# Optimization experiments

Hardware: AMD Instinct MI355X
Metric: run time of the kernel (lower is better)

## Reference

```python
import jax, jax.numpy as jnp
import numpy as np

N_NODES = 100000
N_EDGES = 1600000
IN_F = 128
OUT_F = 32
HEADS = 2
NEG_SLOPE = 0.2  # DGL GATConv default leaky_relu negative slope


def setup_inputs() -> dict:
    key = jax.random.key(0)
    ks = jax.random.split(key, 12)
    x = jax.random.normal(ks[0], (N_NODES, IN_F), dtype=jnp.float32)
    src = jax.random.randint(ks[1], (N_EDGES,), 0, N_NODES, dtype=jnp.int32)
    dst = jax.random.randint(ks[2], (N_EDGES,), 0, N_NODES, dtype=jnp.int32)
    # GATConv params: fc weight [IN_F, HEADS*OUT_F], attn_l/attn_r [HEADS, OUT_F], bias [HEADS*OUT_F]
    s = 1.0 / np.sqrt(IN_F)
    W = jax.random.normal(ks[3], (IN_F, HEADS * OUT_F), dtype=jnp.float32) * s
    attn_l = jax.random.normal(ks[4], (HEADS, OUT_F), dtype=jnp.float32) * s
    attn_r = jax.random.normal(ks[5], (HEADS, OUT_F), dtype=jnp.float32) * s
    bias_gat = jnp.zeros((HEADS * OUT_F,), dtype=jnp.float32)
    # MLPPredictor: lin1 (2*OUT_F -> OUT_F), lin2 (OUT_F -> 1)
    s1 = 1.0 / np.sqrt(2 * OUT_F)
    W1 = jax.random.normal(ks[6], (2 * OUT_F, OUT_F), dtype=jnp.float32) * s1
    b1 = jnp.zeros((OUT_F,), dtype=jnp.float32)
    s2 = 1.0 / np.sqrt(OUT_F)
    W2 = jax.random.normal(ks[7], (OUT_F, 1), dtype=jnp.float32) * s2
    b2 = jnp.zeros((1,), dtype=jnp.float32)
    return {"x": x, "W": W, "attn_l": attn_l, "attn_r": attn_r,
            "bias_gat": bias_gat, "W1": W1, "b1": b1, "W2": W2, "b2": b2,
            "src": src, "dst": dst}


def _forward(x, W, attn_l, attn_r, bias_gat, W1, b1, W2, b2, src, dst):
    # --- GATConv(in, out, 2 heads) ---
    feat = (x @ W).reshape(N_NODES, HEADS, OUT_F)           # [N,H,F]
    el = jnp.einsum('nhf,hf->nh', feat, attn_l)             # [N,H]
    er = jnp.einsum('nhf,hf->nh', feat, attn_r)             # [N,H]
    e = jax.nn.leaky_relu(el[src] + er[dst], NEG_SLOPE)     # [E,H]
    # edge softmax over incoming edges of each dst node (numerically stable)
    m = jax.ops.segment_max(e, dst, num_segments=N_NODES)   # [N,H]
    ex = jnp.exp(e - m[dst])                                # [E,H]
    denom = jax.ops.segment_sum(ex, dst, num_segments=N_NODES)  # [N,H]
    alpha = ex / denom[dst]                                 # [E,H]
    msg = feat[src] * alpha[:, :, None]                     # [E,H,F]
    rst = jax.ops.segment_sum(msg, dst, num_segments=N_NODES)   # [N,H,F]
    rst = rst + bias_gat.reshape(HEADS, OUT_F)
    h = jax.nn.relu(jnp.mean(rst, axis=1))                  # [N,F]
    # --- MLPPredictor: per-edge concat(src,dst) -> lin1 -> lin2 (no activation) ---
    hcat = jnp.concatenate([h[src], h[dst]], axis=1)        # [E,2F]
    score = (hcat @ W1 + b1) @ W2 + b2                      # [E,1]
    return score


def reference(x, W, attn_l, attn_r, bias_gat, W1, b1, W2, b2, src, dst):
    return _forward(x, W, attn_l, attn_r, bias_gat, W1, b1, W2, b2, src, dst)
```

## Files before the change

### kernel.cpp

```cpp
#include <hip/hip_runtime.h>
#include <hip/hip_fp16.h>

#define N_NODES 100000
#define N_EDGES 1600000
#define IN_F 128
#define OUT_F 32
#define HEADS 2
#define HO 64

#define NBUCK 782
#define BIN_BLOCKS 200
#define BIN_THREADS 1024
#define EPB (N_EDGES / BIN_BLOCKS)
#define CAP 36
#define LCAPH 1216

typedef __attribute__((ext_vector_type(8))) _Float16 half8;
typedef __attribute__((ext_vector_type(4))) _Float16 half4v;
typedef __attribute__((ext_vector_type(4))) float    f32x4;

#define XPAD 136

__global__ void wprep_k(const float* __restrict__ W,
                        const float* __restrict__ W1, const float* __restrict__ b1,
                        const float* __restrict__ W2, const float* __restrict__ b2,
                        _Float16* __restrict__ Wt16, float* __restrict__ wcomb,
                        float* __restrict__ ccomb){
  int tid = threadIdx.x;
  if (tid < HO){
    float a = 0.f;
    for (int k = 0; k < OUT_F; ++k) a = fmaf(W1[tid*OUT_F + k], W2[k], a);
    wcomb[tid] = a;
  }
  if (tid == HO){
    float a = 0.f;
    for (int k = 0; k < OUT_F; ++k) a = fmaf(b1[k], W2[k], a);
    *ccomb = a + b2[0];
  }
  for (int i = tid; i < 2048; i += 256){
    int k  = i >> 4;
    int c4 = (i & 15) * 4;
    float4 v = ((const float4*)W)[i];
    Wt16[(c4+0)*IN_F + k] = (_Float16)v.x;
    Wt16[(c4+1)*IN_F + k] = (_Float16)v.y;
    Wt16[(c4+2)*IN_F + k] = (_Float16)v.z;
    Wt16[(c4+3)*IN_F + k] = (_Float16)v.w;
  }
}

__global__ __launch_bounds__(256) void feat_k(
                       const float* __restrict__ x, const _Float16* __restrict__ Wt16,
                       const float* __restrict__ attn_l, const float* __restrict__ attn_r,
                       __half* __restrict__ feat16, float* __restrict__ el, float* __restrict__ er){
  __shared__ __align__(16) _Float16 Ws[64*XPAD];
  __shared__ __align__(16) _Float16 xs[64*XPAD];
  int tid = threadIdx.x;
  int node0 = blockIdx.x*64;

  for (int i = tid; i < 2048; i += 256){
    int c = i >> 5, k4 = i & 31;
    *(uint2*)&Ws[c*XPAD + k4*4] = ((const uint2*)Wt16)[i];
  }
  for (int i = tid; i < 2048; i += 256){
    int ln = i >> 5, kq = i & 31;
    int n = node0 + ln;
    float4 v = (n < N_NODES) ? ((const float4*)x)[(size_t)n*32 + kq]
                             : make_float4(0.f,0.f,0.f,0.f);
    half4v hv = { (_Float16)v.x, (_Float16)v.y, (_Float16)v.z, (_Float16)v.w };
    *(half4v*)&xs[ln*XPAD + kq*4] = hv;
  }
  __syncthreads();

  int w = tid >> 6, lane = tid & 63;
  int row_base = w*16;
  int lr = lane & 15, lg = lane >> 4;
  f32x4 acc0 = {0.f,0.f,0.f,0.f}, acc1 = {0.f,0.f,0.f,0.f};
  f32x4 acc2 = {0.f,0.f,0.f,0.f}, acc3 = {0.f,0.f,0.f,0.f};

  #pragma unroll
  for (int kk = 0; kk < 4; ++kk){
    int ko = kk*32 + lg*8;
    half8 a  = *(const half8*)&xs[(row_base + lr)*XPAD + ko];
    half8 b0 = *(const half8*)&Ws[( 0 + lr)*XPAD + ko];
    half8 b1 = *(const half8*)&Ws[(16 + lr)*XPAD + ko];
    half8 b2 = *(const half8*)&Ws[(32 + lr)*XPAD + ko];
    half8 b3 = *(const half8*)&Ws[(48 + lr)*XPAD + ko];
    acc0 = __builtin_amdgcn_mfma_f32_16x16x32_f16(a, b0, acc0, 0, 0, 0);
    acc1 = __builtin_amdgcn_mfma_f32_16x16x32_f16(a, b1, acc1, 0, 0, 0);
    acc2 = __builtin_amdgcn_mfma_f32_16x16x32_f16(a, b2, acc2, 0, 0, 0);
    acc3 = __builtin_amdgcn_mfma_f32_16x16x32_f16(a, b3, acc3, 0, 0, 0);
  }

  float al0 = attn_l[ 0 + lr], al1 = attn_l[16 + lr];
  float al2 = attn_l[32 + lr], al3 = attn_l[48 + lr];
  float ar0 = attn_r[ 0 + lr], ar1 = attn_r[16 + lr];
  float ar2 = attn_r[32 + lr], ar3 = attn_r[48 + lr];

  #pragma unroll
  for (int r = 0; r < 4; ++r){
    int n = node0 + row_base + lg*4 + r;
    float f0 = acc0[r], f1 = acc1[r], f2 = acc2[r], f3 = acc3[r];
    float p0 = f0*al0 + f1*al1, p1 = f2*al2 + f3*al3;
    float q0 = f0*ar0 + f1*ar1, q1 = f2*ar2 + f3*ar3;
    #pragma unroll
    for (int off = 1; off < 16; off <<= 1){
      p0 += __shfl_xor(p0, off); p1 += __shfl_xor(p1, off);
      q0 += __shfl_xor(q0, off); q1 += __shfl_xor(q1, off);
    }
    if (n < N_NODES){
      size_t base = (size_t)n*HO;
      feat16[base +  0 + lr] = __float2half_rn(f0);
      feat16[base + 16 + lr] = __float2half_rn(f1);
      feat16[base + 32 + lr] = __float2half_rn(f2);
      feat16[base + 48 + lr] = __float2half_rn(f3);
      if (lr == 0){
        *(float2*)&el[n*HEADS] = make_float2(p0, p1);
        *(float2*)&er[n*HEADS] = make_float2(q0, q1);
      }
    }
  }
}

__global__ void bin_k(const int* __restrict__ src, const int* __restrict__ dst,
                      const float* __restrict__ el, const float* __restrict__ er,
                      int* __restrict__ counts_t, uint2* __restrict__ stg){
  __shared__ int cnt[NBUCK];
  int tid = threadIdx.x, blk = blockIdx.x;
  for (int i = tid; i < NBUCK; i += BIN_THREADS) cnt[i] = 0;
  __syncthreads();
  const int4* s4p = (const int4*)(src + blk*EPB);
  const int4* d4p = (const int4*)(dst + blk*EPB);
  for (int i = tid; i < EPB/4; i += BIN_THREADS){
    int4 s4 = s4p[i];
    int4 d4 = d4p[i];
    int ss[4] = {s4.x, s4.y, s4.z, s4.w};
    int dd[4] = {d4.x, d4.y, d4.z, d4.w};
    #pragma unroll
    for (int u = 0; u < 4; ++u){
      int s = ss[u], d = dd[u];
      float2 elv = *(const float2*)&el[s*HEADS];
      float2 erv = *(const float2*)&er[d*HEADS];
      float t0 = elv.x + erv.x, t1 = elv.y + erv.y;
      t0 = t0 > 0.f ? t0 : 0.2f*t0;
      t1 = t1 > 0.f ? t1 : 0.2f*t1;
      __half2 ex2 = __float22half2_rn(make_float2(__expf(t0), __expf(t1)));
      int b = d >> 7;
      int slot = atomicAdd(&cnt[b], 1);
      if (slot < CAP)
        stg[((size_t)blk*NBUCK + b)*CAP + slot] =
          make_uint2(((unsigned int)s << 7) | (unsigned int)(d & 127),
                     *(const unsigned int*)&ex2);
    }
  }
  __syncthreads();
  for (int i = tid; i < NBUCK; i += BIN_THREADS)
    counts_t[i*BIN_BLOCKS + blk] = cnt[i] < CAP ? cnt[i] : CAP;
}

__global__ void __launch_bounds__(512, 8) scatter_agg_k(
                              const int* __restrict__ counts_t, const uint2* __restrict__ stg,
                              const __half* __restrict__ feat16, const float* __restrict__ bias,
                              const float* __restrict__ wcomb,
                              float* __restrict__ s1, float* __restrict__ s2){
  __shared__ uint2 lsev[LCAPH];
  __shared__ int cnts[BIN_BLOCKS];
  __shared__ int hist[64];
  __shared__ int start[64];
  __shared__ int cur[64];
  int bh = blockIdx.x;
  int b = bh >> 1, half = bh & 1;
  int tid = threadIdx.x;
  int w = tid >> 6, lane = tid & 63;
  if (tid < 64) hist[tid] = 0;
  for (int i = tid; i < BIN_BLOCKS; i += 512) cnts[i] = counts_t[b*BIN_BLOCKS + i];
  __syncthreads();

  int grp = tid >> 3, gl = tid & 7;

  for (int sg = grp; sg < BIN_BLOCKS; sg += 64){
    int n_seg = cnts[sg];
    const unsigned int* segx = (const unsigned int*)(stg + ((size_t)sg*NBUCK + b)*CAP);
    for (int j = gl; j < n_seg; j += 8){
      unsigned int rx = segx[2*j];
      int dl = rx & 127;
      if ((dl >> 6) == half) atomicAdd(&hist[dl & 63], 1);
    }
  }
  __syncthreads();

  if (tid < 64){
    int v = hist[tid];
    int inc = v;
    #pragma unroll
    for (int off = 1; off < 64; off <<= 1){
      int t = __shfl_up(inc, off);
      if (lane >= off) inc += t;
    }
    start[tid] = inc - v;
    cur[tid] = inc - v;
  }
  __syncthreads();

  for (int sg = grp; sg < BIN_BLOCKS; sg += 64){
    int n_seg = cnts[sg];
    const uint2* seg = stg + ((size_t)sg*NBUCK + b)*CAP;
    for (int j = gl; j < n_seg; j += 8){
      uint2 r = seg[j];
      int dl = r.x & 127;
      if ((dl >> 6) == half){
        int pos = atomicAdd(&cur[dl & 63], 1);
        if (pos < LCAPH) lsev[pos] = make_uint2(r.x >> 7, r.y);
      }
    }
  }
  __syncthreads();

  int g  = lane >> 4;
  int c4 = lane & 15;
  int h  = (c4 >= 8);
  float b0v = bias[c4*4 + 0], b1v = bias[c4*4 + 1], b2v = bias[c4*4 + 2], b3v = bias[c4*4 + 3];
  int f0 = (c4 & 7)*4;
  int wo = (h ? 32 : 0) + f0;
  float m0 = wcomb[wo], m1 = wcomb[wo+1], m2 = wcomb[wo+2], m3 = wcomb[wo+3];
  for (int i = 0; i < 8; ++i){
    int nl = w*8 + i;
    int node = bh*64 + nl;
    if (node >= N_NODES) break;
    int s0 = start[nl];
    int e0 = cur[nl]; if (e0 > LCAPH) e0 = LCAPH;
    int deg = e0 - s0; if (deg < 0) deg = 0;

    float a0=0.f, a1=0.f, a2=0.f, a3=0.f, dn=0.f;
    for (int j0 = 0; j0 < deg; j0 += 16){
      int jA = j0 + g, jB = j0 + 4 + g, jC = j0 + 8 + g, jD = j0 + 12 + g;
      float alA=0.f, alB=0.f, alC=0.f, alD=0.f;
      int snA=0, snB=0, snC=0, snD=0;
      if (jA < deg){ uint2 r = lsev[s0+jA]; snA = r.x;
        float2 e = __half22float2(*(const __half2*)&r.y); alA = (h?e.y:e.x); }
      if (jB < deg){ uint2 r = lsev[s0+jB]; snB = r.x;
        float2 e = __half22float2(*(const __half2*)&r.y); alB = (h?e.y:e.x); }
      if (jC < deg){ uint2 r = lsev[s0+jC]; snC = r.x;
        float2 e = __half22float2(*(const __half2*)&r.y); alC = (h?e.y:e.x); }
      if (jD < deg){ uint2 r = lsev[s0+jD]; snD = r.x;
        float2 e = __half22float2(*(const __half2*)&r.y); alD = (h?e.y:e.x); }
      dn += alA + alB + alC + alD;
      uint2 vA = *(const uint2*)(feat16 + (size_t)snA*HO + c4*4);
      uint2 vB = *(const uint2*)(feat16 + (size_t)snB*HO + c4*4);
      uint2 vC = *(const uint2*)(feat16 + (size_t)snC*HO + c4*4);
      uint2 vD = *(const uint2*)(feat16 + (size_t)snD*HO + c4*4);
      float2 fA01 = __half22float2(*(const __half2*)&vA.x);
      float2 fA23 = __half22float2(*(const __half2*)&vA.y);
      float2 fB01 = __half22float2(*(const __half2*)&vB.x);
      float2 fB23 = __half22float2(*(const __half2*)&vB.y);
      float2 fC01 = __half22float2(*(const __half2*)&vC.x);
      float2 fC23 = __half22float2(*(const __half2*)&vC.y);
      float2 fD01 = __half22float2(*(const __half2*)&vD.x);
      float2 fD23 = __half22float2(*(const __half2*)&vD.y);
      a0 = fmaf(alA, fA01.x, a0); a0 = fmaf(alB, fB01.x, a0);
      a0 = fmaf(alC, fC01.x, a0); a0 = fmaf(alD, fD01.x, a0);
      a1 = fmaf(alA, fA01.y, a1); a1 = fmaf(alB, fB01.y, a1);
      a1 = fmaf(alC, fC01.y, a1); a1 = fmaf(alD, fD01.y, a1);
      a2 = fmaf(alA, fA23.x, a2); a2 = fmaf(alB, fB23.x, a2);
      a2 = fmaf(alC, fC23.x, a2); a2 = fmaf(alD, fD23.x, a2);
      a3 = fmaf(alA, fA23.y, a3); a3 = fmaf(alB, fB23.y, a3);
      a3 = fmaf(alC, fC23.y, a3); a3 = fmaf(alD, fD23.y, a3);
    }
    a0 += __shfl_xor(a0, 16); a1 += __shfl_xor(a1, 16);
    a2 += __shfl_xor(a2, 16); a3 += __shfl_xor(a3, 16);
    dn += __shfl_xor(dn, 16);
    a0 += __shfl_xor(a0, 32); a1 += __shfl_xor(a1, 32);
    a2 += __shfl_xor(a2, 32); a3 += __shfl_xor(a3, 32);
    dn += __shfl_xor(dn, 32);
    float rh = dn > 0.f ? 1.f/dn : 0.f;
    a0 = fmaf(a0, rh, b0v); a1 = fmaf(a1, rh, b1v);
    a2 = fmaf(a2, rh, b2v); a3 = fmaf(a3, rh, b3v);
    float h0 = 0.5f*(a0 + __shfl_xor(a0, 8)); h0 = fmaxf(h0, 0.f);
    float h1 = 0.5f*(a1 + __shfl_xor(a1, 8)); h1 = fmaxf(h1, 0.f);
    float h2 = 0.5f*(a2 + __shfl_xor(a2, 8)); h2 = fmaxf(h2, 0.f);
    float h3 = 0.5f*(a3 + __shfl_xor(a3, 8)); h3 = fmaxf(h3, 0.f);
    float r = h0*m0 + h1*m1 + h2*m2 + h3*m3;
    r += __shfl_xor(r, 4); r += __shfl_xor(r, 2); r += __shfl_xor(r, 1);
    if (lane == 0)      s1[node] = r;
    else if (lane == 8) s2[node] = r;
  }
}

__global__ void edge_score_k(const int* __restrict__ src, const int* __restrict__ dst,
                             const float* __restrict__ s1, const float* __restrict__ s2,
                             const float* __restrict__ ccomb, float* __restrict__ out){
  int i = blockIdx.x*blockDim.x + threadIdx.x;
  if (i >= N_EDGES/4) return;
  int4 s4 = ((const int4*)src)[i];
  int4 d4 = ((const int4*)dst)[i];
  float c = ccomb[0];
  float4 o;
  o.x = s1[s4.x] + s2[d4.x] + c;
  o.y = s1[s4.y] + s2[d4.y] + c;
  o.z = s1[s4.z] + s2[d4.z] + c;
  o.w = s1[s4.w] + s2[d4.w] + c;
  ((float4*)out)[i] = o;
}

extern "C" void kernel_launch(void* const* d_in, const int* in_sizes, int n_in,
                              void* d_out, int out_size, void* d_ws, size_t ws_size,
                              hipStream_t stream){
  const float* x      = (const float*)d_in[0];
  const float* W      = (const float*)d_in[1];
  const float* attn_l = (const float*)d_in[2];
  const float* attn_r = (const float*)d_in[3];
  const float* bias   = (const float*)d_in[4];
  const float* W1     = (const float*)d_in[5];
  const float* b1     = (const float*)d_in[6];
  const float* W2     = (const float*)d_in[7];
  const float* b2     = (const float*)d_in[8];
  const int*   src    = (const int*)d_in[9];
  const int*   dst    = (const int*)d_in[10];
  float* out = (float*)d_out;

  float* ws = (float*)d_ws;
  size_t off = 0;
  __half* feat16 = (__half*)(ws + off); off += (size_t)N_NODES*HO/2;
  float*  el     = ws + off; off += (size_t)N_NODES*HEADS;
  float*  er     = ws + off; off += (size_t)N_NODES*HEADS;
  float*  s1     = ws + off; off += N_NODES;
  float*  s2     = ws + off; off += N_NODES;
  float*  wcomb  = ws + off; off += 64;
  float*  ccomb  = ws + off; off += 64;
  _Float16* Wt16 = (_Float16*)(ws + off); off += (size_t)HO*IN_F/2;
  int*    counts_t = (int*)(ws + off); off += (size_t)NBUCK*BIN_BLOCKS;
  off = (off + 1) & ~(size_t)1;
  uint2*  stg    = (uint2*)(ws + off); off += (size_t)2*BIN_BLOCKS*NBUCK*CAP;

  wprep_k<<<1, 256, 0, stream>>>(W, W1, b1, W2, b2, Wt16, wcomb, ccomb);
  feat_k<<<(N_NODES + 63)/64, 256, 0, stream>>>(x, Wt16, attn_l, attn_r, feat16, el, er);
  bin_k<<<BIN_BLOCKS, BIN_THREADS, 0, stream>>>(src, dst, el, er, counts_t, stg);
  scatter_agg_k<<<2*NBUCK, 512, 0, stream>>>(counts_t, stg, feat16, bias, wcomb, s1, s2);
  edge_score_k<<<(N_EDGES/4 + 255)/256, 256, 0, stream>>>(src, dst, s1, s2, ccomb, out);
}
```

Baseline: 243.1 us.

## Replace fixed-capacity padded edge staging with exact counting-sort via prefix scan

Edge binning now uses a counting pass and a global prefix scan, so every edge lands in a dense slot of a compact staging array. Previously each bin block had fixed-capacity padded slots. Buckets shrink to 64 nodes, so each aggregation block reads one contiguous range. It no longer scans 200 padded segments and filters half of them. This also removes silent edge dropping at the old per-segment capacity. The cost is two extra kernel launches and an extra full read of dst.

```diff
diff --git a/kernel.cpp b/kernel.cpp
--- a/kernel.cpp
+++ b/kernel.cpp
@@ -8,11 +8,13 @@
 #define HEADS 2
 #define HO 64
 
-#define NBUCK 782
+#define NBUCK2 1563
 #define BIN_BLOCKS 200
 #define BIN_THREADS 1024
 #define EPB (N_EDGES / BIN_BLOCKS)
-#define CAP 36
+#define SCAN_CHUNK 8192
+#define SCAN_M (NBUCK2*BIN_BLOCKS)
+#define SCAN_BLOCKS 39
 #define LCAPH 1216
 
 typedef __attribute__((ext_vector_type(8))) _Float16 half8;
@@ -121,12 +123,88 @@
   }
 }
 
-__global__ void bin_k(const int* __restrict__ src, const int* __restrict__ dst,
+__global__ __launch_bounds__(1024) void binA_k(const int* __restrict__ dst,
+                                               int* __restrict__ counts){
+  __shared__ int cnt[NBUCK2];
+  int tid = threadIdx.x, blk = blockIdx.x;
+  for (int i = tid; i < NBUCK2; i += BIN_THREADS) cnt[i] = 0;
+  __syncthreads();
+  const int4* d4p = (const int4*)(dst + blk*EPB);
+  for (int i = tid; i < EPB/4; i += BIN_THREADS){
+    int4 d4 = d4p[i];
+    atomicAdd(&cnt[d4.x >> 6], 1);
+    atomicAdd(&cnt[d4.y >> 6], 1);
+    atomicAdd(&cnt[d4.z >> 6], 1);
+    atomicAdd(&cnt[d4.w >> 6], 1);
+  }
+  __syncthreads();
+  for (int i = tid; i < NBUCK2; i += BIN_THREADS)
+    counts[i*BIN_BLOCKS + blk] = cnt[i];
+}
+
+__global__ __launch_bounds__(1024) void scanA_k(int* __restrict__ data,
+                                                int* __restrict__ blocksum){
+  __shared__ int wtot[16];
+  int t = threadIdx.x, blk = blockIdx.x;
+  int lane = t & 63, w = t >> 6;
+  int base = blk*SCAN_CHUNK + t*8;
+  int v[8];
+  #pragma unroll
+  for (int u = 0; u < 8; ++u) v[u] = (base+u < SCAN_M) ? data[base+u] : 0;
+  int s = 0;
+  #pragma unroll
+  for (int u = 0; u < 8; ++u){ int t0 = v[u]; v[u] = s; s += t0; }
+  int inc = s;
+  #pragma unroll
+  for (int off = 1; off < 64; off <<= 1){
+    int tt = __shfl_up(inc, off);
+    if (lane >= off) inc += tt;
+  }
+  if (lane == 63) wtot[w] = inc;
+  __syncthreads();
+  if (t < 16){
+    int x = wtot[t];
+    int inc2 = x;
+    #pragma unroll
+    for (int off = 1; off < 16; off <<= 1){
+      int tt = __shfl_up(inc2, off);
+      if (lane >= off) inc2 += tt;
+    }
+    wtot[t] = inc2 - x;
+  }
+  __syncthreads();
+  int myoff = wtot[w] + (inc - s);
+  #pragma unroll
+  for (int u = 0; u < 8; ++u)
+    if (base+u < SCAN_M) data[base+u] = myoff + v[u];
+  if (t == 1023) blocksum[blk] = wtot[15] + inc;
+}
+
+__global__ __launch_bounds__(1024) void binB_k(const int* __restrict__ src,
+                      const int* __restrict__ dst,
                       const float* __restrict__ el, const float* __restrict__ er,
-                      int* __restrict__ counts_t, uint2* __restrict__ stg){
-  __shared__ int cnt[NBUCK];
+                      const int* __restrict__ flatoff, const int* __restrict__ blocksum,
+                      uint2* __restrict__ stg){
+  __shared__ int base_bb[NBUCK2];
+  __shared__ int cnt[NBUCK2];
+  __shared__ int bb[64];
   int tid = threadIdx.x, blk = blockIdx.x;
-  for (int i = tid; i < NBUCK; i += BIN_THREADS) cnt[i] = 0;
+  if (tid < 64){
+    int x = (tid < SCAN_BLOCKS) ? blocksum[tid] : 0;
+    int inc = x;
+    #pragma unroll
+    for (int off = 1; off < 64; off <<= 1){
+      int tt = __shfl_up(inc, off);
+      if ((tid & 63) >= off) inc += tt;
+    }
+    bb[tid] = inc - x;
+  }
+  __syncthreads();
+  for (int i = tid; i < NBUCK2; i += BIN_THREADS){
+    int fi = i*BIN_BLOCKS + blk;
+    base_bb[i] = flatoff[fi] + bb[fi >> 13];
+    cnt[i] = 0;
+  }
   __syncthreads();
   const int4* s4p = (const int4*)(src + blk*EPB);
   const int4* d4p = (const int4*)(dst + blk*EPB);
@@ -144,48 +222,56 @@
       t0 = t0 > 0.f ? t0 : 0.2f*t0;
       t1 = t1 > 0.f ? t1 : 0.2f*t1;
       __half2 ex2 = __float22half2_rn(make_float2(__expf(t0), __expf(t1)));
-      int b = d >> 7;
-      int slot = atomicAdd(&cnt[b], 1);
-      if (slot < CAP)
-        stg[((size_t)blk*NBUCK + b)*CAP + slot] =
-          make_uint2(((unsigned int)s << 7) | (unsigned int)(d & 127),
-                     *(const unsigned int*)&ex2);
-    }
-  }
-  __syncthreads();
-  for (int i = tid; i < NBUCK; i += BIN_THREADS)
-    counts_t[i*BIN_BLOCKS + blk] = cnt[i] < CAP ? cnt[i] : CAP;
+      int b = d >> 6;
+      int slot = base_bb[b] + atomicAdd(&cnt[b], 1);
+      stg[slot] = make_uint2(((unsigned int)s << 6) | (unsigned int)(d & 63),
+                             *(const unsigned int*)&ex2);
+    }
+  }
 }
 
 __global__ void __launch_bounds__(512, 8) scatter_agg_k(
-                              const int* __restrict__ counts_t, const uint2* __restrict__ stg,
+                              const int* __restrict__ flatoff, const int* __restrict__ blocksum,
+                              const uint2* __restrict__ stg,
                               const __half* __restrict__ feat16, const float* __restrict__ bias,
                               const float* __restrict__ wcomb,
                               float* __restrict__ s1, float* __restrict__ s2){
   __shared__ uint2 lsev[LCAPH];
-  __shared__ int cnts[BIN_BLOCKS];
   __shared__ int hist[64];
-  __shared__ int start[64];
+  __shared__ int start_[64];
   __shared__ int cur[64];
-  int bh = blockIdx.x;
-  int b = bh >> 1, half = bh & 1;
+  __shared__ int bb[64];
+  __shared__ int range[2];
+  int b = blockIdx.x;
   int tid = threadIdx.x;
   int w = tid >> 6, lane = tid & 63;
-  if (tid < 64) hist[tid] = 0;
-  for (int i = tid; i < BIN_BLOCKS; i += 512) cnts[i] = counts_t[b*BIN_BLOCKS + i];
-  __syncthreads();
-
-  int grp = tid >> 3, gl = tid & 7;
-
-  for (int sg = grp; sg < BIN_BLOCKS; sg += 64){
-    int n_seg = cnts[sg];
-    const unsigned int* segx = (const unsigned int*)(stg + ((size_t)sg*NBUCK + b)*CAP);
-    for (int j = gl; j < n_seg; j += 8){
-      unsigned int rx = segx[2*j];
-      int dl = rx & 127;
-      if ((dl >> 6) == half) atomicAdd(&hist[dl & 63], 1);
-    }
-  }
+  if (tid < 64){
+    hist[tid] = 0;
+    int x = (tid < SCAN_BLOCKS) ? blocksum[tid] : 0;
+    int inc = x;
+    #pragma unroll
+    for (int off = 1; off < 64; off <<= 1){
+      int tt = __shfl_up(inc, off);
+      if (lane >= off) inc += tt;
+    }
+    bb[tid] = inc - x;
+  }
+  __syncthreads();
+  if (tid == 0){
+    int fi = b*BIN_BLOCKS;
+    int rs = flatoff[fi] + bb[fi >> 13];
+    int re;
+    if (b == NBUCK2-1) re = N_EDGES;
+    else { int fj = (b+1)*BIN_BLOCKS; re = flatoff[fj] + bb[fj >> 13]; }
+    range[0] = rs; range[1] = re;
+  }
+  __syncthreads();
+  int rs = range[0];
+  int nrec = range[1] - rs;
+  const uint2* rec = stg + rs;
+
+  for (int j = tid; j < nrec; j += 512)
+    atomicAdd(&hist[rec[j].x & 63], 1);
   __syncthreads();
 
   if (tid < 64){
@@ -196,22 +282,15 @@
       int t = __shfl_up(inc, off);
       if (lane >= off) inc += t;
     }
-    start[tid] = inc - v;
+    start_[tid] = inc - v;
     cur[tid] = inc - v;
   }
   __syncthreads();
 
-  for (int sg = grp; sg < BIN_BLOCKS; sg += 64){
-    int n_seg = cnts[sg];
-    const uint2* seg = stg + ((size_t)sg*NBUCK + b)*CAP;
-    for (int j = gl; j < n_seg; j += 8){
-      uint2 r = seg[j];
-      int dl = r.x & 127;
-      if ((dl >> 6) == half){
-        int pos = atomicAdd(&cur[dl & 63], 1);
-        if (pos < LCAPH) lsev[pos] = make_uint2(r.x >> 7, r.y);
-      }
-    }
+  for (int j = tid; j < nrec; j += 512){
+    uint2 r = rec[j];
+    int pos = atomicAdd(&cur[r.x & 63], 1);
+    if (pos < LCAPH) lsev[pos] = make_uint2(r.x >> 6, r.y);
   }
   __syncthreads();
 
@@ -224,9 +303,9 @@
   float m0 = wcomb[wo], m1 = wcomb[wo+1], m2 = wcomb[wo+2], m3 = wcomb[wo+3];
   for (int i = 0; i < 8; ++i){
     int nl = w*8 + i;
-    int node = bh*64 + nl;
+    int node = b*64 + nl;
     if (node >= N_NODES) break;
-    int s0 = start[nl];
+    int s0 = start_[nl];
     int e0 = cur[nl]; if (e0 > LCAPH) e0 = LCAPH;
     int deg = e0 - s0; if (deg < 0) deg = 0;
 
@@ -327,13 +406,16 @@
   float*  wcomb  = ws + off; off += 64;
   float*  ccomb  = ws + off; off += 64;
   _Float16* Wt16 = (_Float16*)(ws + off); off += (size_t)HO*IN_F/2;
-  int*    counts_t = (int*)(ws + off); off += (size_t)NBUCK*BIN_BLOCKS;
+  int*    flatoff  = (int*)(ws + off); off += (size_t)SCAN_M;
+  int*    blocksum = (int*)(ws + off); off += 64;
   off = (off + 1) & ~(size_t)1;
-  uint2*  stg    = (uint2*)(ws + off); off += (size_t)2*BIN_BLOCKS*NBUCK*CAP;
-
+  uint2*  stg    = (uint2*)(ws + off); off += (size_t)2*N_EDGES;
+
+  binA_k<<<BIN_BLOCKS, BIN_THREADS, 0, stream>>>(dst, flatoff);
+  scanA_k<<<SCAN_BLOCKS, 1024, 0, stream>>>(flatoff, blocksum);
   wprep_k<<<1, 256, 0, stream>>>(W, W1, b1, W2, b2, Wt16, wcomb, ccomb);
   feat_k<<<(N_NODES + 63)/64, 256, 0, stream>>>(x, Wt16, attn_l, attn_r, feat16, el, er);
-  bin_k<<<BIN_BLOCKS, BIN_THREADS, 0, stream>>>(src, dst, el, er, counts_t, stg);
-  scatter_agg_k<<<2*NBUCK, 512, 0, stream>>>(counts_t, stg, feat16, bias, wcomb, s1, s2);
+  binB_k<<<BIN_BLOCKS, BIN_THREADS, 0, stream>>>(src, dst, el, er, flatoff, blocksum, stg);
+  scatter_agg_k<<<NBUCK2, 512, 0, stream>>>(flatoff, blocksum, stg, feat16, bias, wcomb, s1, s2);
   edge_score_k<<<(N_EDGES/4 + 255)/256, 256, 0, stream>>>(src, dst, s1, s2, ccomb, out);
 }
```

Measured after the change: 236.9 us. -2.6%, faster.

## Replace fixed-capacity edge bins with exact counting-sort bins and drop weight-prep kernel

Applied to the files above, without the earlier changes.

The binning kernel now holds each thread's edges in registers, counts per 64-node bucket, runs a prefix scan and writes a compact, exactly sized per-block bucketed staging array with offsets. The old design used padded capacity slots and two-way halves. The aggregation kernel reads only its own bucket's edges, with no half filtering, and launches one block per 64 nodes. The separate weight-prep kernel is removed: W is transposed inside feat_k, the combined MLP weights are computed per block, and the bias constant is computed in the binning kernel. This removes one launch, the wasted reads of padded slots and the risk of dropping edges when a slot overflows, at the cost of a second atomic pass and redundant per-block weight work.

```diff
diff --git a/kernel.cpp b/kernel.cpp
--- a/kernel.cpp
+++ b/kernel.cpp
@@ -8,11 +8,11 @@
 #define HEADS 2
 #define HO 64
 
-#define NBUCK 782
-#define BIN_BLOCKS 200
+#define NBUCK2 1563
+#define BIN_BLOCKS 256
 #define BIN_THREADS 1024
 #define EPB (N_EDGES / BIN_BLOCKS)
-#define CAP 36
+#define NPT 7
 #define LCAPH 1216
 
 typedef __attribute__((ext_vector_type(8))) _Float16 half8;
@@ -21,35 +21,8 @@
 
 #define XPAD 136
 
-__global__ void wprep_k(const float* __restrict__ W,
-                        const float* __restrict__ W1, const float* __restrict__ b1,
-                        const float* __restrict__ W2, const float* __restrict__ b2,
-                        _Float16* __restrict__ Wt16, float* __restrict__ wcomb,
-                        float* __restrict__ ccomb){
-  int tid = threadIdx.x;
-  if (tid < HO){
-    float a = 0.f;
-    for (int k = 0; k < OUT_F; ++k) a = fmaf(W1[tid*OUT_F + k], W2[k], a);
-    wcomb[tid] = a;
-  }
-  if (tid == HO){
-    float a = 0.f;
-    for (int k = 0; k < OUT_F; ++k) a = fmaf(b1[k], W2[k], a);
-    *ccomb = a + b2[0];
-  }
-  for (int i = tid; i < 2048; i += 256){
-    int k  = i >> 4;
-    int c4 = (i & 15) * 4;
-    float4 v = ((const float4*)W)[i];
-    Wt16[(c4+0)*IN_F + k] = (_Float16)v.x;
-    Wt16[(c4+1)*IN_F + k] = (_Float16)v.y;
-    Wt16[(c4+2)*IN_F + k] = (_Float16)v.z;
-    Wt16[(c4+3)*IN_F + k] = (_Float16)v.w;
-  }
-}
-
 __global__ __launch_bounds__(256) void feat_k(
-                       const float* __restrict__ x, const _Float16* __restrict__ Wt16,
+                       const float* __restrict__ x, const float* __restrict__ W,
                        const float* __restrict__ attn_l, const float* __restrict__ attn_r,
                        __half* __restrict__ feat16, float* __restrict__ el, float* __restrict__ er){
   __shared__ __align__(16) _Float16 Ws[64*XPAD];
@@ -58,8 +31,12 @@
   int node0 = blockIdx.x*64;
 
   for (int i = tid; i < 2048; i += 256){
-    int c = i >> 5, k4 = i & 31;
-    *(uint2*)&Ws[c*XPAD + k4*4] = ((const uint2*)Wt16)[i];
+    int k = i >> 4, c4 = (i & 15)*4;
+    float4 v = ((const float4*)W)[i];
+    Ws[(c4+0)*XPAD + k] = (_Float16)v.x;
+    Ws[(c4+1)*XPAD + k] = (_Float16)v.y;
+    Ws[(c4+2)*XPAD + k] = (_Float16)v.z;
+    Ws[(c4+3)*XPAD + k] = (_Float16)v.w;
   }
   for (int i = tid; i < 2048; i += 256){
     int ln = i >> 5, kq = i & 31;
@@ -121,70 +98,115 @@
   }
 }
 
-__global__ void bin_k(const int* __restrict__ src, const int* __restrict__ dst,
+__global__ __launch_bounds__(1024) void binB_k(const int* __restrict__ src,
+                      const int* __restrict__ dst,
                       const float* __restrict__ el, const float* __restrict__ er,
-                      int* __restrict__ counts_t, uint2* __restrict__ stg){
-  __shared__ int cnt[NBUCK];
+                      const float* __restrict__ b1, const float* __restrict__ W2,
+                      const float* __restrict__ b2,
+                      int* __restrict__ bstart, float* __restrict__ ccomb,
+                      uint2* __restrict__ stg){
+  __shared__ int cnt[NBUCK2];
   int tid = threadIdx.x, blk = blockIdx.x;
-  for (int i = tid; i < NBUCK; i += BIN_THREADS) cnt[i] = 0;
-  __syncthreads();
-  const int4* s4p = (const int4*)(src + blk*EPB);
-  const int4* d4p = (const int4*)(dst + blk*EPB);
-  for (int i = tid; i < EPB/4; i += BIN_THREADS){
-    int4 s4 = s4p[i];
-    int4 d4 = d4p[i];
-    int ss[4] = {s4.x, s4.y, s4.z, s4.w};
-    int dd[4] = {d4.x, d4.y, d4.z, d4.w};
-    #pragma unroll
-    for (int u = 0; u < 4; ++u){
-      int s = ss[u], d = dd[u];
+  int lane = tid & 63, w = tid >> 6;
+  if (blk == 0 && tid == 0){
+    float a = 0.f;
+    for (int k = 0; k < OUT_F; ++k) a = fmaf(b1[k], W2[k], a);
+    *ccomb = a + b2[0];
+  }
+  for (int i = tid; i < NBUCK2; i += BIN_THREADS) cnt[i] = 0;
+  __syncthreads();
+
+  unsigned rx[NPT], rex[NPT];
+  int rb[NPT];
+  int ebase = blk*EPB;
+  #pragma unroll
+  for (int u = 0; u < NPT; ++u){
+    int idx = tid + u*BIN_THREADS;
+    rb[u] = -1;
+    if (idx < EPB){
+      int s = src[ebase + idx];
+      int d = dst[ebase + idx];
       float2 elv = *(const float2*)&el[s*HEADS];
       float2 erv = *(const float2*)&er[d*HEADS];
       float t0 = elv.x + erv.x, t1 = elv.y + erv.y;
       t0 = t0 > 0.f ? t0 : 0.2f*t0;
       t1 = t1 > 0.f ? t1 : 0.2f*t1;
       __half2 ex2 = __float22half2_rn(make_float2(__expf(t0), __expf(t1)));
-      int b = d >> 7;
-      int slot = atomicAdd(&cnt[b], 1);
-      if (slot < CAP)
-        stg[((size_t)blk*NBUCK + b)*CAP + slot] =
-          make_uint2(((unsigned int)s << 7) | (unsigned int)(d & 127),
-                     *(const unsigned int*)&ex2);
-    }
-  }
-  __syncthreads();
-  for (int i = tid; i < NBUCK; i += BIN_THREADS)
-    counts_t[i*BIN_BLOCKS + blk] = cnt[i] < CAP ? cnt[i] : CAP;
+      int b = d >> 6;
+      rb[u] = b;
+      rx[u] = ((unsigned)s << 6) | (unsigned)(d & 63);
+      rex[u] = *(const unsigned*)&ex2;
+      atomicAdd(&cnt[b], 1);
+    }
+  }
+  __syncthreads();
+
+  if (w == 0){
+    int run = 0;
+    for (int c = 0; c < NBUCK2; c += 64){
+      int i = c + lane;
+      int v = (i < NBUCK2) ? cnt[i] : 0;
+      int inc = v;
+      #pragma unroll
+      for (int off = 1; off < 64; off <<= 1){
+        int t = __shfl_up(inc, off);
+        if (lane >= off) inc += t;
+      }
+      if (i < NBUCK2) cnt[i] = run + inc - v;
+      run += __shfl(inc, 63);
+    }
+  }
+  __syncthreads();
+
+  for (int i = tid; i < NBUCK2; i += BIN_THREADS)
+    bstart[(size_t)blk*NBUCK2 + i] = cnt[i];
+  __syncthreads();
+
+  #pragma unroll
+  for (int u = 0; u < NPT; ++u){
+    if (rb[u] >= 0){
+      int pos = atomicAdd(&cnt[rb[u]], 1);
+      stg[(size_t)blk*EPB + pos] = make_uint2(rx[u], rex[u]);
+    }
+  }
 }
 
 __global__ void __launch_bounds__(512, 8) scatter_agg_k(
-                              const int* __restrict__ counts_t, const uint2* __restrict__ stg,
+                              const int* __restrict__ bstart, const uint2* __restrict__ stg,
                               const __half* __restrict__ feat16, const float* __restrict__ bias,
-                              const float* __restrict__ wcomb,
+                              const float* __restrict__ W1, const float* __restrict__ W2,
                               float* __restrict__ s1, float* __restrict__ s2){
   __shared__ uint2 lsev[LCAPH];
-  __shared__ int cnts[BIN_BLOCKS];
+  __shared__ int soff[BIN_BLOCKS];
+  __shared__ int send[BIN_BLOCKS];
+  __shared__ float wc[64];
   __shared__ int hist[64];
-  __shared__ int start[64];
+  __shared__ int start_[64];
   __shared__ int cur[64];
-  int bh = blockIdx.x;
-  int b = bh >> 1, half = bh & 1;
+  int b = blockIdx.x;
   int tid = threadIdx.x;
   int w = tid >> 6, lane = tid & 63;
-  if (tid < 64) hist[tid] = 0;
-  for (int i = tid; i < BIN_BLOCKS; i += 512) cnts[i] = counts_t[b*BIN_BLOCKS + i];
+  if (tid < 64){
+    hist[tid] = 0;
+    float a = 0.f;
+    #pragma unroll
+    for (int k = 0; k < OUT_F; ++k) a = fmaf(W1[tid*OUT_F + k], W2[k], a);
+    wc[tid] = a;
+  }
+  for (int i = tid; i < BIN_BLOCKS; i += 512){
+    int o = bstart[(size_t)i*NBUCK2 + b];
+    int e = (b == NBUCK2-1) ? EPB : bstart[(size_t)i*NBUCK2 + b + 1];
+    soff[i] = o; send[i] = e;
+  }
   __syncthreads();
 
   int grp = tid >> 3, gl = tid & 7;
 
   for (int sg = grp; sg < BIN_BLOCKS; sg += 64){
-    int n_seg = cnts[sg];
-    const unsigned int* segx = (const unsigned int*)(stg + ((size_t)sg*NBUCK + b)*CAP);
-    for (int j = gl; j < n_seg; j += 8){
-      unsigned int rx = segx[2*j];
-      int dl = rx & 127;
-      if ((dl >> 6) == half) atomicAdd(&hist[dl & 63], 1);
-    }
+    const uint2* seg = stg + (size_t)sg*EPB;
+    int e = send[sg];
+    for (int j = soff[sg] + gl; j < e; j += 8)
+      atomicAdd(&hist[seg[j].x & 63], 1);
   }
   __syncthreads();
 
@@ -196,21 +218,18 @@
       int t = __shfl_up(inc, off);
       if (lane >= off) inc += t;
     }
-    start[tid] = inc - v;
+    start_[tid] = inc - v;
     cur[tid] = inc - v;
   }
   __syncthreads();
 
   for (int sg = grp; sg < BIN_BLOCKS; sg += 64){
-    int n_seg = cnts[sg];
-    const uint2* seg = stg + ((size_t)sg*NBUCK + b)*CAP;
-    for (int j = gl; j < n_seg; j += 8){
+    const uint2* seg = stg + (size_t)sg*EPB;
+    int e = send[sg];
+    for (int j = soff[sg] + gl; j < e; j += 8){
       uint2 r = seg[j];
-      int dl = r.x & 127;
-      if ((dl >> 6) == half){
-        int pos = atomicAdd(&cur[dl & 63], 1);
-        if (pos < LCAPH) lsev[pos] = make_uint2(r.x >> 7, r.y);
-      }
+      int pos = atomicAdd(&cur[r.x & 63], 1);
+      if (pos < LCAPH) lsev[pos] = make_uint2(r.x >> 6, r.y);
     }
   }
   __syncthreads();
@@ -221,12 +240,12 @@
   float b0v = bias[c4*4 + 0], b1v = bias[c4*4 + 1], b2v = bias[c4*4 + 2], b3v = bias[c4*4 + 3];
   int f0 = (c4 & 7)*4;
   int wo = (h ? 32 : 0) + f0;
-  float m0 = wcomb[wo], m1 = wcomb[wo+1], m2 = wcomb[wo+2], m3 = wcomb[wo+3];
+  float m0 = wc[wo], m1 = wc[wo+1], m2 = wc[wo+2], m3 = wc[wo+3];
   for (int i = 0; i < 8; ++i){
     int nl = w*8 + i;
-    int node = bh*64 + nl;
+    int node = b*64 + nl;
     if (node >= N_NODES) break;
-    int s0 = start[nl];
+    int s0 = start_[nl];
     int e0 = cur[nl]; if (e0 > LCAPH) e0 = LCAPH;
     int deg = e0 - s0; if (deg < 0) deg = 0;
 
@@ -324,16 +343,14 @@
   float*  er     = ws + off; off += (size_t)N_NODES*HEADS;
   float*  s1     = ws + off; off += N_NODES;
   float*  s2     = ws + off; off += N_NODES;
-  float*  wcomb  = ws + off; off += 64;
   float*  ccomb  = ws + off; off += 64;
-  _Float16* Wt16 = (_Float16*)(ws + off); off += (size_t)HO*IN_F/2;
-  int*    counts_t = (int*)(ws + off); off += (size_t)NBUCK*BIN_BLOCKS;
+  int*    bstart = (int*)(ws + off); off += (size_t)BIN_BLOCKS*NBUCK2;
   off = (off + 1) & ~(size_t)1;
-  uint2*  stg    = (uint2*)(ws + off); off += (size_t)2*BIN_BLOCKS*NBUCK*CAP;
-
-  wprep_k<<<1, 256, 0, stream>>>(W, W1, b1, W2, b2, Wt16, wcomb, ccomb);
-  feat_k<<<(N_NODES + 63)/64, 256, 0, stream>>>(x, Wt16, attn_l, attn_r, feat16, el, er);
-  bin_k<<<BIN_BLOCKS, BIN_THREADS, 0, stream>>>(src, dst, el, er, counts_t, stg);
-  scatter_agg_k<<<2*NBUCK, 512, 0, stream>>>(counts_t, stg, feat16, bias, wcomb, s1, s2);
+  uint2*  stg    = (uint2*)(ws + off); off += (size_t)2*N_EDGES;
+
+  feat_k<<<(N_NODES + 63)/64, 256, 0, stream>>>(x, W, attn_l, attn_r, feat16, el, er);
+  binB_k<<<BIN_BLOCKS, BIN_THREADS, 0, stream>>>(src, dst, el, er, b1, W2, b2,
+                                                 bstart, ccomb, stg);
+  scatter_agg_k<<<NBUCK2, 512, 0, stream>>>(bstart, stg, feat16, bias, W1, W2, s1, s2);
   edge_score_k<<<(N_EDGES/4 + 255)/256, 256, 0, stream>>>(src, dst, s1, s2, ccomb, out);
 }
```

After: 223.3 us. -8.2%, faster.
